# Optimization experiments

Measured on AMD Instinct MI355X. Metric: run time of the kernel, lower is better.

The kernel has to match this reference:

```python
import jax, jax.numpy as jnp
import numpy as np
import math

B, L, D = 4, 4096, 1024
M = 256  # num random features
EPS = 1e-06


def setup_inputs() -> dict:
    key = jax.random.key(0)
    kq, kk, kv, kp = jax.random.split(key, 4)
    Q = jax.random.normal(kq, (B, L, D), dtype=jnp.float32)
    K = jax.random.normal(kk, (B, L, D), dtype=jnp.float32)
    V = jax.random.normal(kv, (B, L, D), dtype=jnp.float32)
    # Gaussian random projection (ortho_features=False path): shape (num_features, d_model)
    projection = jax.random.normal(kp, (M, D), dtype=jnp.float32)
    return {"Q": Q, "K": K, "V": V, "projection": projection}


def reference(Q, K, V, projection):
    d_model = Q.shape[-1]
    m = projection.shape[0]
    inv_sqrt_d = 1.0 / math.sqrt(d_model)
    # random features: exp((x / sqrt(d)) @ P^T)
    rf_q = jnp.exp(jnp.einsum('bld,md->blm', Q * inv_sqrt_d, projection)) / math.sqrt(m)  # (B,L,M)
    rf_k = jnp.exp(jnp.einsum('bld,md->blm', K * inv_sqrt_d, projection))                 # (B,L,M)
    # linear attention: KV state and normalizer
    KV = jnp.einsum('blm,bld->bmd', rf_k, V)   # (B,M,D)
    Z = jnp.sum(rf_k, axis=1)                   # (B,M)
    out = jnp.einsum('blm,bmd->bld', rf_q, KV)  # (B,L,D)
    normalizer = jnp.einsum('blm,bm->bl', rf_q, Z) + EPS  # (B,L)
    return out / normalizer[..., None]
```

## Files before the change

kernel.cpp:

```cpp
#include <hip/hip_runtime.h>
#include <math.h>

#define NB 4
#define LL 4096
#define DD 1024
#define MM 256

typedef short s16x8 __attribute__((ext_vector_type(8)));
typedef short s16x4 __attribute__((ext_vector_type(4)));
typedef float fx4 __attribute__((ext_vector_type(4)));
typedef unsigned u32x2 __attribute__((ext_vector_type(2)));
typedef unsigned u32x4 __attribute__((ext_vector_type(4)));

__device__ __forceinline__ float b2f(short s) {
  union { unsigned u; float f; } v;
  v.u = ((unsigned)(unsigned short)s) << 16;
  return v.f;
}
__device__ __forceinline__ short f2b(float f) {
  union { float f; unsigned u; } v;
  v.f = f;
  unsigned r = (v.u + 0x7fffu + ((v.u >> 16) & 1u)) >> 16;
  return (short)(unsigned short)r;
}
__device__ __forceinline__ unsigned cvt2(float lo, float hi) {
  unsigned r;
  asm("v_cvt_pk_bf16_f32 %0, %1, %2" : "=v"(r) : "v"(lo), "v"(hi));
  return r;
}
__device__ __forceinline__ int swz(int row, int col) {
  return row * 64 + (col ^ ((row & 7) << 3));
}
__device__ __forceinline__ int keyf(int m) { return (m ^ (m >> 2)) & 3; }

typedef __attribute__((address_space(1))) const void* gas1_t;
typedef __attribute__((address_space(3))) void* las3_t;
#define GLL16(g, l) __builtin_amdgcn_global_load_lds((gas1_t)(const void*)(g), (las3_t)(void*)(l), 16, 0, 0)

__global__ __launch_bounds__(256) void k_cast(const float* __restrict__ in, short* __restrict__ out, int n4) {
  int i = blockIdx.x * 256 + threadIdx.x;
  if (i >= n4) return;
  float4 v = ((const float4*)in)[i];
  s16x4 s;
  s[0] = f2b(v.x); s[1] = f2b(v.y); s[2] = f2b(v.z); s[3] = f2b(v.w);
  ((s16x4*)out)[i] = s;
}

__global__ __launch_bounds__(256, 2) void k_qk(const float* __restrict__ Q, const float* __restrict__ K,
                                               const short* __restrict__ Pb,
                                               short* __restrict__ rfq, short* __restrict__ rfkT,
                                               float* __restrict__ Zz) {
  __shared__ short As[2][4096];
  __shared__ short Bs[2][16384];
  int z = blockIdx.z, mode = z >> 2, b = z & 3;
  int l0 = blockIdx.x * 64;
  const float* X = mode ? K : Q;
  int tid = threadIdx.x, lane = tid & 63, w = tid >> 6;
  int m16 = lane & 15, kg = lane >> 4;

  int arow = tid >> 2, acol = (tid & 3) * 16;
  int akey = (arow & 7) << 3;
  const float* Xr = X + ((size_t)b * LL + l0 + arow) * DD + acol;

  fx4 acc[4][4] = {};
  float4 pa[4];

  #pragma unroll
  for (int i = 0; i < 4; ++i) pa[i] = *(const float4*)(Xr + i * 4);
  #pragma unroll
  for (int j = 0; j < 8; ++j) {
    int fl = tid + j * 256, row = fl >> 3, c8 = fl & 7;
    GLL16(Pb + (size_t)row * DD + (c8 ^ (row & 7)) * 8, &Bs[0][fl * 8]);
  }
  {
    u32x4 v0;
    v0[0] = cvt2(pa[0].x, pa[0].y); v0[1] = cvt2(pa[0].z, pa[0].w);
    v0[2] = cvt2(pa[1].x, pa[1].y); v0[3] = cvt2(pa[1].z, pa[1].w);
    *(u32x4*)&As[0][arow * 64 + (acol ^ akey)] = v0;
    v0[0] = cvt2(pa[2].x, pa[2].y); v0[1] = cvt2(pa[2].z, pa[2].w);
    v0[2] = cvt2(pa[3].x, pa[3].y); v0[3] = cvt2(pa[3].z, pa[3].w);
    *(u32x4*)&As[0][arow * 64 + ((acol + 8) ^ akey)] = v0;
  }
  __syncthreads();

  for (int t = 0; t < 16; ++t) {
    int cur = t & 1, nxt = cur ^ 1;
    if (t < 15) {
      int d1 = (t + 1) * 64;
      #pragma unroll
      for (int i = 0; i < 4; ++i) pa[i] = *(const float4*)(Xr + d1 + i * 4);
      #pragma unroll
      for (int j = 0; j < 8; ++j) {
        int fl = tid + j * 256, row = fl >> 3, c8 = fl & 7;
        GLL16(Pb + (size_t)row * DD + d1 + (c8 ^ (row & 7)) * 8, &Bs[nxt][fl * 8]);
      }
    }
    #pragma unroll
    for (int ks = 0; ks < 2; ++ks) {
      int kb = ks * 32 + kg * 8;
      s16x8 af[4], bf[4];
      #pragma unroll
      for (int mi = 0; mi < 4; ++mi) af[mi] = *(const s16x8*)&As[cur][swz(mi * 16 + m16, kb)];
      #pragma unroll
      for (int ni = 0; ni < 4; ++ni) bf[ni] = *(const s16x8*)&Bs[cur][swz(w * 64 + ni * 16 + m16, kb)];
      #pragma unroll
      for (int mi = 0; mi < 4; ++mi)
        #pragma unroll
        for (int ni = 0; ni < 4; ++ni)
          acc[mi][ni] = __builtin_amdgcn_mfma_f32_16x16x32_bf16(af[mi], bf[ni], acc[mi][ni], 0, 0, 0);
    }
    if (t < 15) {
      u32x4 v0;
      v0[0] = cvt2(pa[0].x, pa[0].y); v0[1] = cvt2(pa[0].z, pa[0].w);
      v0[2] = cvt2(pa[1].x, pa[1].y); v0[3] = cvt2(pa[1].z, pa[1].w);
      *(u32x4*)&As[nxt][arow * 64 + (acol ^ akey)] = v0;
      v0[0] = cvt2(pa[2].x, pa[2].y); v0[1] = cvt2(pa[2].z, pa[2].w);
      v0[2] = cvt2(pa[3].x, pa[3].y); v0[3] = cvt2(pa[3].z, pa[3].w);
      *(u32x4*)&As[nxt][arow * 64 + ((acol + 8) ^ akey)] = v0;
    }
    __syncthreads();
  }

  if (mode == 0) {
    #pragma unroll
    for (int mi = 0; mi < 4; ++mi)
      #pragma unroll
      for (int ni = 0; ni < 4; ++ni) {
        int r0 = mi * 16 + (kg << 2);
        int c = w * 64 + ni * 16 + m16;
        #pragma unroll
        for (int u = 0; u < 4; ++u)
          rfq[((size_t)b * LL + l0 + r0 + u) * MM + c] = f2b(expf(acc[mi][ni][u] * 0.03125f) * 0.0625f);
      }
  } else {
    short* T = (short*)Bs;
    float zp[4] = {0.f, 0.f, 0.f, 0.f};
    #pragma unroll
    for (int mi = 0; mi < 4; ++mi)
      #pragma unroll
      for (int ni = 0; ni < 4; ++ni) {
        int l = mi * 16 + (kg << 2);
        int m = w * 64 + ni * 16 + m16;
        int key = (m & 7) << 3;
        float e0 = expf(acc[mi][ni][0] * 0.03125f);
        float e1 = expf(acc[mi][ni][1] * 0.03125f);
        float e2 = expf(acc[mi][ni][2] * 0.03125f);
        float e3 = expf(acc[mi][ni][3] * 0.03125f);
        zp[ni] += e0 + e1 + e2 + e3;
        *(unsigned*)&T[m * 64 + (l ^ key)] = cvt2(e0, e1);
        *(unsigned*)&T[m * 64 + ((l ^ key) + 2)] = cvt2(e2, e3);
      }
    #pragma unroll
    for (int ni = 0; ni < 4; ++ni) {
      zp[ni] += __shfl_xor(zp[ni], 16);
      zp[ni] += __shfl_xor(zp[ni], 32);
    }
    if (kg == 0) {
      #pragma unroll
      for (int ni = 0; ni < 4; ++ni)
        atomicAdd(&Zz[b * MM + w * 64 + ni * 16 + m16], zp[ni]);
    }
    __syncthreads();
    int m = tid, mkey = (m & 7) << 3;
    short* dst = rfkT + ((size_t)b * MM + m) * LL + l0;
    #pragma unroll
    for (int j = 0; j < 8; ++j) {
      s16x8 v = *(const s16x8*)&T[m * 64 + ((j * 8) ^ mkey)];
      *(s16x8*)(dst + j * 8) = v;
    }
  }
}

__global__ __launch_bounds__(512) void k_kv(const float* __restrict__ V, const short* __restrict__ rfkT,
                                            float* __restrict__ KVp) {
  __shared__ float Vs[2][32 * 129];
  __shared__ short Ak[2][256 * 32];
  int d0 = blockIdx.x * 128, kc = blockIdx.y, b = blockIdx.z;
  int ls = kc * 512;
  int tid = threadIdx.x, lane = tid & 63, w = tid >> 6;
  int wm = w >> 1, wd = w & 1;
  int m16 = lane & 15, kg = lane >> 4;

  int vl = tid >> 4, vf = (tid & 15) * 8;
  const float* Vb = V + ((size_t)b * LL + ls + vl) * DD + d0 + vf;

  int am = tid >> 2, as = tid & 3;
  int acs = as ^ keyf(am);
  const short* AkS0 = rfkT + ((size_t)b * MM + am) * LL + ls + acs * 8;
  const short* AkS1 = rfkT + ((size_t)b * MM + am + 128) * LL + ls + acs * 8;

  fx4 acc[4][4] = {};
  float4 pv0, pv1;

  pv0 = *(const float4*)(Vb);
  pv1 = *(const float4*)(Vb + 4);
  GLL16(AkS0, &Ak[0][tid * 8]);
  GLL16(AkS1, &Ak[0][(tid + 512) * 8]);
  #pragma unroll
  for (int j = 0; j < 4; ++j) {
    Vs[0][vl * 129 + vf + j] = ((const float*)&pv0)[j];
    Vs[0][vl * 129 + vf + 4 + j] = ((const float*)&pv1)[j];
  }
  __syncthreads();

  for (int ch = 0; ch < 16; ++ch) {
    int cur = ch & 1, nxt = cur ^ 1;
    if (ch < 15) {
      int lo = (ch + 1) * 32;
      pv0 = *(const float4*)(Vb + (size_t)lo * DD);
      pv1 = *(const float4*)(Vb + (size_t)lo * DD + 4);
      GLL16(AkS0 + lo, &Ak[nxt][tid * 8]);
      GLL16(AkS1 + lo, &Ak[nxt][(tid + 512) * 8]);
    }
    s16x8 af[4];
    #pragma unroll
    for (int mi = 0; mi < 4; ++mi) {
      int m = wm * 64 + mi * 16 + m16;
      af[mi] = *(const s16x8*)&Ak[cur][m * 32 + ((kg ^ keyf(m)) * 8)];
    }
    #pragma unroll
    for (int ni = 0; ni < 4; ++ni) {
      int d = wd * 64 + ni * 16 + m16;
      const float* vs = &Vs[cur][kg * 8 * 129 + d];
      u32x4 bw;
      bw[0] = cvt2(vs[0], vs[129]);
      bw[1] = cvt2(vs[258], vs[387]);
      bw[2] = cvt2(vs[516], vs[645]);
      bw[3] = cvt2(vs[774], vs[903]);
      s16x8 bf = *(s16x8*)&bw;
      #pragma unroll
      for (int mi = 0; mi < 4; ++mi)
        acc[mi][ni] = __builtin_amdgcn_mfma_f32_16x16x32_bf16(af[mi], bf, acc[mi][ni], 0, 0, 0);
    }
    if (ch < 15) {
      #pragma unroll
      for (int j = 0; j < 4; ++j) {
        Vs[nxt][vl * 129 + vf + j] = ((const float*)&pv0)[j];
        Vs[nxt][vl * 129 + vf + 4 + j] = ((const float*)&pv1)[j];
      }
    }
    __syncthreads();
  }

  float* dst = KVp + (((size_t)kc * NB + b) * DD + d0) * MM;
  #pragma unroll
  for (int mi = 0; mi < 4; ++mi)
    #pragma unroll
    for (int ni = 0; ni < 4; ++ni) {
      int d = wd * 64 + ni * 16 + m16;
      int m = wm * 64 + mi * 16 + (kg << 2);
      *(float4*)(dst + (size_t)d * MM + m) = *(float4*)&acc[mi][ni];
    }
}

__global__ __launch_bounds__(256) void k_red(const float* __restrict__ KVp, float* __restrict__ KVTf) {
  int i = blockIdx.x * 256 + threadIdx.x;
  const float4* p = (const float4*)KVp;
  float4 s = p[i];
  #pragma unroll
  for (int k = 1; k < 8; ++k) {
    float4 v = p[i + k * 262144];
    s.x += v.x; s.y += v.y; s.z += v.z; s.w += v.w;
  }
  ((float4*)KVTf)[i] = s;
}

__global__ __launch_bounds__(512) void k_out(const short* __restrict__ rfq, const float* __restrict__ KVTf,
                                             const float* __restrict__ Zz, float* __restrict__ out) {
  __shared__ short Aq[2][8192];
  __shared__ short Bv[2][8192];
  __shared__ float zl[256];
  __shared__ float np[512];
  __shared__ float nf[128];
  int l0 = blockIdx.x * 128, d0 = blockIdx.y * 128, b = blockIdx.z;
  int tid = threadIdx.x, lane = tid & 63, w = tid >> 6;
  int wr = w >> 2, wc = w & 3;
  int brow = tid >> 2, bq = (tid & 3) * 16;
  int bkey = (brow & 7) << 3;
  const float* Kf = KVTf + ((size_t)b * DD + d0 + brow) * MM + bq;
  short* Bw0 = &Bv[0][brow * 64 + (bq ^ bkey)];
  short* Bw1 = &Bv[0][brow * 64 + ((bq + 8) ^ bkey)];
  const short* Ab = rfq + ((size_t)b * LL + l0) * MM;
  int f1 = tid + 512;
  int ar0 = tid >> 3, ac0 = tid & 7, ar1 = f1 >> 3, ac1 = f1 & 7;
  int nrow = tid & 127, nsub = tid >> 7;
  if (tid < 256) zl[tid] = Zz[b * MM + tid];
  fx4 acc[4][2] = {};
  float4 pb[4];
  float na = 0.f;

  #pragma unroll
  for (int i = 0; i < 4; ++i) pb[i] = *(const float4*)(Kf + i * 4);
  GLL16(Ab + (size_t)ar0 * MM + (ac0 ^ (ar0 & 7)) * 8, &Aq[0][tid * 8]);
  GLL16(Ab + (size_t)ar1 * MM + (ac1 ^ (ar1 & 7)) * 8, &Aq[0][f1 * 8]);
  {
    u32x2 v0, v1;
    v0[0] = cvt2(pb[0].x, pb[0].y); v0[1] = cvt2(pb[0].z, pb[0].w);
    v1[0] = cvt2(pb[1].x, pb[1].y); v1[1] = cvt2(pb[1].z, pb[1].w);
    *(u32x2*)Bw0 = v0;
    *(u32x2*)(Bw0 + 4) = v1;
    v0[0] = cvt2(pb[2].x, pb[2].y); v0[1] = cvt2(pb[2].z, pb[2].w);
    v1[0] = cvt2(pb[3].x, pb[3].y); v1[1] = cvt2(pb[3].z, pb[3].w);
    *(u32x2*)Bw1 = v0;
    *(u32x2*)(Bw1 + 4) = v1;
  }
  __syncthreads();

  for (int t = 0; t < 4; ++t) {
    int cur = t & 1, nxt = cur ^ 1;
    int m1 = ((t + 1) & 3) * 64;
    #pragma unroll
    for (int i = 0; i < 4; ++i) pb[i] = *(const float4*)(Kf + m1 + i * 4);
    GLL16(Ab + (size_t)ar0 * MM + m1 + (ac0 ^ (ar0 & 7)) * 8, &Aq[nxt][tid * 8]);
    GLL16(Ab + (size_t)ar1 * MM + m1 + (ac1 ^ (ar1 & 7)) * 8, &Aq[nxt][f1 * 8]);
    #pragma unroll
    for (int kk = 0; kk < 16; ++kk) {
      int k = nsub * 16 + kk;
      na += b2f(Aq[cur][nrow * 64 + (k ^ ((nrow & 7) << 3))]) * zl[t * 64 + k];
    }
    #pragma unroll
    for (int ks = 0; ks < 2; ++ks) {
      int kb = ks * 32 + (lane >> 4) * 8;
      s16x8 af[4], bf[2];
      #pragma unroll
      for (int mi = 0; mi < 4; ++mi) {
        int row = wr * 64 + mi * 16 + (lane & 15);
        af[mi] = *(const s16x8*)&Aq[cur][row * 64 + (kb ^ ((row & 7) << 3))];
      }
      #pragma unroll
      for (int ni = 0; ni < 2; ++ni) {
        int row = wc * 32 + ni * 16 + (lane & 15);
        bf[ni] = *(const s16x8*)&Bv[cur][row * 64 + (kb ^ ((row & 7) << 3))];
      }
      #pragma unroll
      for (int mi = 0; mi < 4; ++mi)
        #pragma unroll
        for (int ni = 0; ni < 2; ++ni)
          acc[mi][ni] = __builtin_amdgcn_mfma_f32_16x16x32_bf16(af[mi], bf[ni], acc[mi][ni], 0, 0, 0);
    }
    {
      u32x2 v0, v1;
      v0[0] = cvt2(pb[0].x, pb[0].y); v0[1] = cvt2(pb[0].z, pb[0].w);
      v1[0] = cvt2(pb[1].x, pb[1].y); v1[1] = cvt2(pb[1].z, pb[1].w);
      *(u32x2*)(Bw0 + nxt * 8192) = v0;
      *(u32x2*)(Bw0 + nxt * 8192 + 4) = v1;
      v0[0] = cvt2(pb[2].x, pb[2].y); v0[1] = cvt2(pb[2].z, pb[2].w);
      v1[0] = cvt2(pb[3].x, pb[3].y); v1[1] = cvt2(pb[3].z, pb[3].w);
      *(u32x2*)(Bw1 + nxt * 8192) = v0;
      *(u32x2*)(Bw1 + nxt * 8192 + 4) = v1;
    }
    __syncthreads();
  }
  np[tid] = na;
  __syncthreads();
  if (tid < 128) nf[tid] = np[tid] + np[tid + 128] + np[tid + 256] + np[tid + 384] + 1e-6f;
  __syncthreads();
  #pragma unroll
  for (int mi = 0; mi < 4; ++mi)
    #pragma unroll
    for (int ni = 0; ni < 2; ++ni) {
      int l = wr * 64 + mi * 16 + ((lane >> 4) << 2);
      int d = d0 + wc * 32 + ni * 16 + (lane & 15);
      #pragma unroll
      for (int u = 0; u < 4; ++u)
        out[((size_t)b * LL + l0 + l + u) * DD + d] = acc[mi][ni][u] / nf[l + u];
    }
}

extern "C" void kernel_launch(void* const* d_in, const int* in_sizes, int n_in,
                              void* d_out, int out_size, void* d_ws, size_t ws_size,
                              hipStream_t stream) {
  const float* Q = (const float*)d_in[0];
  const float* K = (const float*)d_in[1];
  const float* V = (const float*)d_in[2];
  const float* P = (const float*)d_in[3];
  float* out = (float*)d_out;
  char* ws = (char*)d_ws;

  short* Pb   = (short*)(ws + 0);
  float* Zz   = (float*)(ws + 524288);
  float* KVTf = (float*)(ws + 528384);
  short* rfq  = (short*)(ws + 4722688);
  short* rfkT = (short*)(ws + 13111296);
  float* KVp  = (float*)(ws + 21499904);

  k_cast<<<256, 256, 0, stream>>>(P, Pb, 65536);
  (void)hipMemsetAsync(Zz, 0, 4096, stream);
  k_qk<<<dim3(64, 1, 2 * NB), 256, 0, stream>>>(Q, K, Pb, rfq, rfkT, Zz);
  k_kv<<<dim3(8, 8, NB), 512, 0, stream>>>(V, rfkT, KVp);
  k_red<<<1024, 256, 0, stream>>>(KVp, KVTf);
  k_out<<<dim3(32, 8, NB), 512, 0, stream>>>(rfq, KVTf, Zz, out);
}
```

Baseline: 137.4 us.

## Restructure QK projection kernel into 256-wide X chunks with finer P double-buffering

The X (Q/K) tile is now loaded in four chunks of 256 columns, each held in registers (16 float4 per thread), converted to bf16 and stored once into a larger swizzled LDS buffer. The projection tile is streamed in 32-wide k-steps with double-buffered global-to-LDS loads and a new XOR swizzle. The aim is fewer X-load/barrier rounds and bigger, more latency-tolerant global loads. In exchange it adds more barriers per k-step, higher register pressure from 64 float registers, and no overlap of the X loads with MFMA work at chunk boundaries.

```diff
diff --git a/kernel.cpp b/kernel.cpp
--- a/kernel.cpp
+++ b/kernel.cpp
@@ -27,9 +27,6 @@
   unsigned r;
   asm("v_cvt_pk_bf16_f32 %0, %1, %2" : "=v"(r) : "v"(lo), "v"(hi));
   return r;
-}
-__device__ __forceinline__ int swz(int row, int col) {
-  return row * 64 + (col ^ ((row & 7) << 3));
 }
 __device__ __forceinline__ int keyf(int m) { return (m ^ (m >> 2)) & 3; }
 
@@ -50,75 +47,70 @@
                                                const short* __restrict__ Pb,
                                                short* __restrict__ rfq, short* __restrict__ rfkT,
                                                float* __restrict__ Zz) {
-  __shared__ short As[2][4096];
-  __shared__ short Bs[2][16384];
+  __shared__ short As[64 * 256];
+  __shared__ short Bs[2][8192];
   int z = blockIdx.z, mode = z >> 2, b = z & 3;
   int l0 = blockIdx.x * 64;
   const float* X = mode ? K : Q;
   int tid = threadIdx.x, lane = tid & 63, w = tid >> 6;
   int m16 = lane & 15, kg = lane >> 4;
 
-  int arow = tid >> 2, acol = (tid & 3) * 16;
-  int akey = (arow & 7) << 3;
-  const float* Xr = X + ((size_t)b * LL + l0 + arow) * DD + acol;
+  int arow = tid >> 2, acol = (tid & 3) * 64;
+  int akey = (arow & 7) << 4;
+  char* Asb = (char*)As + arow * 512;
 
   fx4 acc[4][4] = {};
-  float4 pa[4];
-
-  #pragma unroll
-  for (int i = 0; i < 4; ++i) pa[i] = *(const float4*)(Xr + i * 4);
-  #pragma unroll
-  for (int j = 0; j < 8; ++j) {
-    int fl = tid + j * 256, row = fl >> 3, c8 = fl & 7;
-    GLL16(Pb + (size_t)row * DD + (c8 ^ (row & 7)) * 8, &Bs[0][fl * 8]);
-  }
-  {
-    u32x4 v0;
-    v0[0] = cvt2(pa[0].x, pa[0].y); v0[1] = cvt2(pa[0].z, pa[0].w);
-    v0[2] = cvt2(pa[1].x, pa[1].y); v0[3] = cvt2(pa[1].z, pa[1].w);
-    *(u32x4*)&As[0][arow * 64 + (acol ^ akey)] = v0;
-    v0[0] = cvt2(pa[2].x, pa[2].y); v0[1] = cvt2(pa[2].z, pa[2].w);
-    v0[2] = cvt2(pa[3].x, pa[3].y); v0[3] = cvt2(pa[3].z, pa[3].w);
-    *(u32x4*)&As[0][arow * 64 + ((acol + 8) ^ akey)] = v0;
-  }
-  __syncthreads();
-
-  for (int t = 0; t < 16; ++t) {
-    int cur = t & 1, nxt = cur ^ 1;
-    if (t < 15) {
-      int d1 = (t + 1) * 64;
-      #pragma unroll
-      for (int i = 0; i < 4; ++i) pa[i] = *(const float4*)(Xr + d1 + i * 4);
-      #pragma unroll
-      for (int j = 0; j < 8; ++j) {
-        int fl = tid + j * 256, row = fl >> 3, c8 = fl & 7;
-        GLL16(Pb + (size_t)row * DD + d1 + (c8 ^ (row & 7)) * 8, &Bs[nxt][fl * 8]);
-      }
-    }
-    #pragma unroll
-    for (int ks = 0; ks < 2; ++ks) {
-      int kb = ks * 32 + kg * 8;
+
+  for (int c = 0; c < 4; ++c) {
+    if (c) __syncthreads();
+    const float* Xc = X + ((size_t)b * LL + l0 + arow) * DD + c * 256 + acol;
+    float4 pa[16];
+    #pragma unroll
+    for (int i = 0; i < 16; ++i) pa[i] = *(const float4*)(Xc + i * 4);
+    #pragma unroll
+    for (int j = 0; j < 4; ++j) {
+      int fl = tid + j * 256, m = fl >> 2, ch = fl & 3;
+      GLL16(Pb + (size_t)m * DD + c * 256 + (ch ^ keyf(m)) * 8, &Bs[0][fl * 8]);
+    }
+    #pragma unroll
+    for (int i = 0; i < 8; ++i) {
+      u32x4 v;
+      v[0] = cvt2(pa[2 * i].x, pa[2 * i].y);
+      v[1] = cvt2(pa[2 * i].z, pa[2 * i].w);
+      v[2] = cvt2(pa[2 * i + 1].x, pa[2 * i + 1].y);
+      v[3] = cvt2(pa[2 * i + 1].z, pa[2 * i + 1].w);
+      int colb = (tid & 3) * 128 + i * 16;
+      *(u32x4*)(Asb + (colb ^ akey)) = v;
+    }
+    __syncthreads();
+    for (int s = 0; s < 8; ++s) {
+      int buf = s & 1;
+      if (s < 7) {
+        #pragma unroll
+        for (int j = 0; j < 4; ++j) {
+          int fl = tid + j * 256, m = fl >> 2, ch = fl & 3;
+          GLL16(Pb + (size_t)m * DD + c * 256 + (s + 1) * 32 + (ch ^ keyf(m)) * 8, &Bs[buf ^ 1][fl * 8]);
+        }
+      }
       s16x8 af[4], bf[4];
-      #pragma unroll
-      for (int mi = 0; mi < 4; ++mi) af[mi] = *(const s16x8*)&As[cur][swz(mi * 16 + m16, kb)];
-      #pragma unroll
-      for (int ni = 0; ni < 4; ++ni) bf[ni] = *(const s16x8*)&Bs[cur][swz(w * 64 + ni * 16 + m16, kb)];
+      int colb = s * 64 + kg * 16;
+      #pragma unroll
+      for (int mi = 0; mi < 4; ++mi) {
+        int row = mi * 16 + m16;
+        af[mi] = *(const s16x8*)((const char*)As + row * 512 + (colb ^ ((row & 7) << 4)));
+      }
+      #pragma unroll
+      for (int ni = 0; ni < 4; ++ni) {
+        int m = w * 64 + ni * 16 + m16;
+        bf[ni] = *(const s16x8*)&Bs[buf][m * 32 + (kg ^ keyf(m)) * 8];
+      }
       #pragma unroll
       for (int mi = 0; mi < 4; ++mi)
         #pragma unroll
         for (int ni = 0; ni < 4; ++ni)
           acc[mi][ni] = __builtin_amdgcn_mfma_f32_16x16x32_bf16(af[mi], bf[ni], acc[mi][ni], 0, 0, 0);
-    }
-    if (t < 15) {
-      u32x4 v0;
-      v0[0] = cvt2(pa[0].x, pa[0].y); v0[1] = cvt2(pa[0].z, pa[0].w);
-      v0[2] = cvt2(pa[1].x, pa[1].y); v0[3] = cvt2(pa[1].z, pa[1].w);
-      *(u32x4*)&As[nxt][arow * 64 + (acol ^ akey)] = v0;
-      v0[0] = cvt2(pa[2].x, pa[2].y); v0[1] = cvt2(pa[2].z, pa[2].w);
-      v0[2] = cvt2(pa[3].x, pa[3].y); v0[3] = cvt2(pa[3].z, pa[3].w);
-      *(u32x4*)&As[nxt][arow * 64 + ((acol + 8) ^ akey)] = v0;
-    }
-    __syncthreads();
+      if (s < 7) __syncthreads();
+    }
   }
 
   if (mode == 0) {
@@ -133,6 +125,7 @@
           rfq[((size_t)b * LL + l0 + r0 + u) * MM + c] = f2b(expf(acc[mi][ni][u] * 0.03125f) * 0.0625f);
       }
   } else {
+    __syncthreads();
     short* T = (short*)Bs;
     float zp[4] = {0.f, 0.f, 0.f, 0.f};
     #pragma unroll
```

Measured after the change: 146.0 us. 6.2% more time.

## Halve k_kv tile width, emit bf16 KV from reduction, async-load KV in k_out

Applied to the files above, without the earlier changes.

k_kv now uses 64-wide d tiles, which doubles the grid to 512 blocks, and asks for 4 blocks per CU through its launch bounds, for better occupancy. It also fixes the swizzle key for the second half of the rows. k_red converts the reduced KV state to bf16 before storing it. This halves the bytes written and read, and lets k_out stage KV with direct global-to-LDS loads instead of register float loads plus conversion. k_out also stops issuing a wasted prefetch on its last iteration. The cost is extra redundant rfkT loads in k_kv, plus one extra bf16 rounding step, which replaces the rounding k_out already did.

```diff
diff --git a/kernel.cpp b/kernel.cpp
--- a/kernel.cpp
+++ b/kernel.cpp
@@ -171,44 +171,38 @@
   }
 }
 
-__global__ __launch_bounds__(512) void k_kv(const float* __restrict__ V, const short* __restrict__ rfkT,
-                                            float* __restrict__ KVp) {
-  __shared__ float Vs[2][32 * 129];
+__global__ __launch_bounds__(512, 4) void k_kv(const float* __restrict__ V, const short* __restrict__ rfkT,
+                                               float* __restrict__ KVp) {
+  __shared__ float Vs[2][32 * 65];
   __shared__ short Ak[2][256 * 32];
-  int d0 = blockIdx.x * 128, kc = blockIdx.y, b = blockIdx.z;
+  int d0 = blockIdx.x * 64, kc = blockIdx.y, b = blockIdx.z;
   int ls = kc * 512;
   int tid = threadIdx.x, lane = tid & 63, w = tid >> 6;
   int wm = w >> 1, wd = w & 1;
   int m16 = lane & 15, kg = lane >> 4;
 
-  int vl = tid >> 4, vf = (tid & 15) * 8;
+  int vl = tid >> 4, vf = (tid & 15) * 4;
   const float* Vb = V + ((size_t)b * LL + ls + vl) * DD + d0 + vf;
 
   int am = tid >> 2, as = tid & 3;
-  int acs = as ^ keyf(am);
-  const short* AkS0 = rfkT + ((size_t)b * MM + am) * LL + ls + acs * 8;
-  const short* AkS1 = rfkT + ((size_t)b * MM + am + 128) * LL + ls + acs * 8;
-
-  fx4 acc[4][4] = {};
-  float4 pv0, pv1;
-
-  pv0 = *(const float4*)(Vb);
-  pv1 = *(const float4*)(Vb + 4);
+  const short* AkS0 = rfkT + ((size_t)b * MM + am) * LL + ls + (as ^ keyf(am)) * 8;
+  const short* AkS1 = rfkT + ((size_t)b * MM + am + 128) * LL + ls + (as ^ keyf(am + 128)) * 8;
+
+  fx4 acc[4][2] = {};
+  float4 pv;
+
+  pv = *(const float4*)(Vb);
   GLL16(AkS0, &Ak[0][tid * 8]);
   GLL16(AkS1, &Ak[0][(tid + 512) * 8]);
   #pragma unroll
-  for (int j = 0; j < 4; ++j) {
-    Vs[0][vl * 129 + vf + j] = ((const float*)&pv0)[j];
-    Vs[0][vl * 129 + vf + 4 + j] = ((const float*)&pv1)[j];
-  }
+  for (int j = 0; j < 4; ++j) Vs[0][vl * 65 + vf + j] = ((const float*)&pv)[j];
   __syncthreads();
 
   for (int ch = 0; ch < 16; ++ch) {
     int cur = ch & 1, nxt = cur ^ 1;
     if (ch < 15) {
       int lo = (ch + 1) * 32;
-      pv0 = *(const float4*)(Vb + (size_t)lo * DD);
-      pv1 = *(const float4*)(Vb + (size_t)lo * DD + 4);
+      pv = *(const float4*)(Vb + (size_t)lo * DD);
       GLL16(AkS0 + lo, &Ak[nxt][tid * 8]);
       GLL16(AkS1 + lo, &Ak[nxt][(tid + 512) * 8]);
     }
@@ -219,14 +213,14 @@
       af[mi] = *(const s16x8*)&Ak[cur][m * 32 + ((kg ^ keyf(m)) * 8)];
     }
     #pragma unroll
-    for (int ni = 0; ni < 4; ++ni) {
-      int d = wd * 64 + ni * 16 + m16;
-      const float* vs = &Vs[cur][kg * 8 * 129 + d];
+    for (int ni = 0; ni < 2; ++ni) {
+      int d = wd * 32 + ni * 16 + m16;
+      const float* vs = &Vs[cur][kg * 8 * 65 + d];
       u32x4 bw;
-      bw[0] = cvt2(vs[0], vs[129]);
-      bw[1] = cvt2(vs[258], vs[387]);
-      bw[2] = cvt2(vs[516], vs[645]);
-      bw[3] = cvt2(vs[774], vs[903]);
+      bw[0] = cvt2(vs[0], vs[65]);
+      bw[1] = cvt2(vs[130], vs[195]);
+      bw[2] = cvt2(vs[260], vs[325]);
+      bw[3] = cvt2(vs[390], vs[455]);
       s16x8 bf = *(s16x8*)&bw;
       #pragma unroll
       for (int mi = 0; mi < 4; ++mi)
@@ -234,10 +228,7 @@
     }
     if (ch < 15) {
       #pragma unroll
-      for (int j = 0; j < 4; ++j) {
-        Vs[nxt][vl * 129 + vf + j] = ((const float*)&pv0)[j];
-        Vs[nxt][vl * 129 + vf + 4 + j] = ((const float*)&pv1)[j];
-      }
+      for (int j = 0; j < 4; ++j) Vs[nxt][vl * 65 + vf + j] = ((const float*)&pv)[j];
     }
     __syncthreads();
   }
@@ -246,14 +237,14 @@
   #pragma unroll
   for (int mi = 0; mi < 4; ++mi)
     #pragma unroll
-    for (int ni = 0; ni < 4; ++ni) {
-      int d = wd * 64 + ni * 16 + m16;
+    for (int ni = 0; ni < 2; ++ni) {
+      int d = wd * 32 + ni * 16 + m16;
       int m = wm * 64 + mi * 16 + (kg << 2);
       *(float4*)(dst + (size_t)d * MM + m) = *(float4*)&acc[mi][ni];
     }
 }
 
-__global__ __launch_bounds__(256) void k_red(const float* __restrict__ KVp, float* __restrict__ KVTf) {
+__global__ __launch_bounds__(256) void k_red(const float* __restrict__ KVp, short* __restrict__ KVTb) {
   int i = blockIdx.x * 256 + threadIdx.x;
   const float4* p = (const float4*)KVp;
   float4 s = p[i];
@@ -262,10 +253,13 @@
     float4 v = p[i + k * 262144];
     s.x += v.x; s.y += v.y; s.z += v.z; s.w += v.w;
   }
-  ((float4*)KVTf)[i] = s;
-}
-
-__global__ __launch_bounds__(512) void k_out(const short* __restrict__ rfq, const float* __restrict__ KVTf,
+  u32x2 o;
+  o[0] = cvt2(s.x, s.y);
+  o[1] = cvt2(s.z, s.w);
+  ((u32x2*)KVTb)[i] = o;
+}
+
+__global__ __launch_bounds__(512) void k_out(const short* __restrict__ rfq, const short* __restrict__ KVTb,
                                              const float* __restrict__ Zz, float* __restrict__ out) {
   __shared__ short Aq[2][8192];
   __shared__ short Bv[2][8192];
@@ -275,44 +269,30 @@
   int l0 = blockIdx.x * 128, d0 = blockIdx.y * 128, b = blockIdx.z;
   int tid = threadIdx.x, lane = tid & 63, w = tid >> 6;
   int wr = w >> 2, wc = w & 3;
-  int brow = tid >> 2, bq = (tid & 3) * 16;
-  int bkey = (brow & 7) << 3;
-  const float* Kf = KVTf + ((size_t)b * DD + d0 + brow) * MM + bq;
-  short* Bw0 = &Bv[0][brow * 64 + (bq ^ bkey)];
-  short* Bw1 = &Bv[0][brow * 64 + ((bq + 8) ^ bkey)];
   const short* Ab = rfq + ((size_t)b * LL + l0) * MM;
+  const short* Bb = KVTb + ((size_t)b * DD + d0) * MM;
   int f1 = tid + 512;
   int ar0 = tid >> 3, ac0 = tid & 7, ar1 = f1 >> 3, ac1 = f1 & 7;
   int nrow = tid & 127, nsub = tid >> 7;
   if (tid < 256) zl[tid] = Zz[b * MM + tid];
   fx4 acc[4][2] = {};
-  float4 pb[4];
   float na = 0.f;
 
-  #pragma unroll
-  for (int i = 0; i < 4; ++i) pb[i] = *(const float4*)(Kf + i * 4);
   GLL16(Ab + (size_t)ar0 * MM + (ac0 ^ (ar0 & 7)) * 8, &Aq[0][tid * 8]);
   GLL16(Ab + (size_t)ar1 * MM + (ac1 ^ (ar1 & 7)) * 8, &Aq[0][f1 * 8]);
-  {
-    u32x2 v0, v1;
-    v0[0] = cvt2(pb[0].x, pb[0].y); v0[1] = cvt2(pb[0].z, pb[0].w);
-    v1[0] = cvt2(pb[1].x, pb[1].y); v1[1] = cvt2(pb[1].z, pb[1].w);
-    *(u32x2*)Bw0 = v0;
-    *(u32x2*)(Bw0 + 4) = v1;
-    v0[0] = cvt2(pb[2].x, pb[2].y); v0[1] = cvt2(pb[2].z, pb[2].w);
-    v1[0] = cvt2(pb[3].x, pb[3].y); v1[1] = cvt2(pb[3].z, pb[3].w);
-    *(u32x2*)Bw1 = v0;
-    *(u32x2*)(Bw1 + 4) = v1;
-  }
+  GLL16(Bb + (size_t)ar0 * MM + (ac0 ^ (ar0 & 7)) * 8, &Bv[0][tid * 8]);
+  GLL16(Bb + (size_t)ar1 * MM + (ac1 ^ (ar1 & 7)) * 8, &Bv[0][f1 * 8]);
   __syncthreads();
 
   for (int t = 0; t < 4; ++t) {
     int cur = t & 1, nxt = cur ^ 1;
-    int m1 = ((t + 1) & 3) * 64;
-    #pragma unroll
-    for (int i = 0; i < 4; ++i) pb[i] = *(const float4*)(Kf + m1 + i * 4);
-    GLL16(Ab + (size_t)ar0 * MM + m1 + (ac0 ^ (ar0 & 7)) * 8, &Aq[nxt][tid * 8]);
-    GLL16(Ab + (size_t)ar1 * MM + m1 + (ac1 ^ (ar1 & 7)) * 8, &Aq[nxt][f1 * 8]);
+    if (t < 3) {
+      int m1 = (t + 1) * 64;
+      GLL16(Ab + (size_t)ar0 * MM + m1 + (ac0 ^ (ar0 & 7)) * 8, &Aq[nxt][tid * 8]);
+      GLL16(Ab + (size_t)ar1 * MM + m1 + (ac1 ^ (ar1 & 7)) * 8, &Aq[nxt][f1 * 8]);
+      GLL16(Bb + (size_t)ar0 * MM + m1 + (ac0 ^ (ar0 & 7)) * 8, &Bv[nxt][tid * 8]);
+      GLL16(Bb + (size_t)ar1 * MM + m1 + (ac1 ^ (ar1 & 7)) * 8, &Bv[nxt][f1 * 8]);
+    }
     #pragma unroll
     for (int kk = 0; kk < 16; ++kk) {
       int k = nsub * 16 + kk;
@@ -337,17 +317,6 @@
         #pragma unroll
         for (int ni = 0; ni < 2; ++ni)
           acc[mi][ni] = __builtin_amdgcn_mfma_f32_16x16x32_bf16(af[mi], bf[ni], acc[mi][ni], 0, 0, 0);
-    }
-    {
-      u32x2 v0, v1;
-      v0[0] = cvt2(pb[0].x, pb[0].y); v0[1] = cvt2(pb[0].z, pb[0].w);
-      v1[0] = cvt2(pb[1].x, pb[1].y); v1[1] = cvt2(pb[1].z, pb[1].w);
-      *(u32x2*)(Bw0 + nxt * 8192) = v0;
-      *(u32x2*)(Bw0 + nxt * 8192 + 4) = v1;
-      v0[0] = cvt2(pb[2].x, pb[2].y); v0[1] = cvt2(pb[2].z, pb[2].w);
-      v1[0] = cvt2(pb[3].x, pb[3].y); v1[1] = cvt2(pb[3].z, pb[3].w);
-      *(u32x2*)(Bw1 + nxt * 8192) = v0;
-      *(u32x2*)(Bw1 + nxt * 8192 + 4) = v1;
     }
     __syncthreads();
   }
@@ -379,7 +348,7 @@
 
   short* Pb   = (short*)(ws + 0);
   float* Zz   = (float*)(ws + 524288);
-  float* KVTf = (float*)(ws + 528384);
+  short* KVTb = (short*)(ws + 528384);
   short* rfq  = (short*)(ws + 4722688);
   short* rfkT = (short*)(ws + 13111296);
   float* KVp  = (float*)(ws + 21499904);
@@ -387,7 +356,7 @@
   k_cast<<<256, 256, 0, stream>>>(P, Pb, 65536);
   (void)hipMemsetAsync(Zz, 0, 4096, stream);
   k_qk<<<dim3(64, 1, 2 * NB), 256, 0, stream>>>(Q, K, Pb, rfq, rfkT, Zz);
-  k_kv<<<dim3(8, 8, NB), 512, 0, stream>>>(V, rfkT, KVp);
-  k_red<<<1024, 256, 0, stream>>>(KVp, KVTf);
-  k_out<<<dim3(32, 8, NB), 512, 0, stream>>>(rfq, KVTf, Zz, out);
-}
+  k_kv<<<dim3(16, 8, NB), 512, 0, stream>>>(V, rfkT, KVp);
+  k_red<<<1024, 256, 0, stream>>>(KVp, KVTb);
+  k_out<<<dim3(32, 8, NB), 512, 0, stream>>>(rfq, KVTb, Zz, out);
+}
```

Measured after the change: 126.9 us. 7.7% less time.
